# Kernel tuning notes

Hardware: AMD Instinct MI355X
Metric: run time of the kernel (lower is better)

Reference implementation:

```python
import jax, jax.numpy as jnp
import numpy as np

B, S, IN, H, Z = 8, 128, 64, 128, 64
N0, N1, N2 = B * S * S, B * (S // 2) ** 2, B * (S // 4) ** 2


def _grid(side, nb):
    # 4-neighbor grid, both edge directions, for nb stacked graphs
    idx = np.arange(side * side).reshape(side, side)
    h = np.stack([idx[:, :-1].ravel(), idx[:, 1:].ravel()])
    v = np.stack([idx[:-1, :].ravel(), idx[1:, :].ravel()])
    e = np.concatenate([h, v, h[::-1], v[::-1]], axis=1)  # [2, 4*side*(side-1)]
    return np.concatenate([e + g * side * side for g in range(nb)], axis=1)


def _cluster(side, nb):
    # 2x2 block clustering: (i,j) -> (i//2, j//2) on each graph
    i, j = np.meshgrid(np.arange(side), np.arange(side), indexing='ij')
    c = ((i // 2) * (side // 2) + (j // 2)).ravel()
    return np.concatenate([c + g * (side // 2) ** 2 for g in range(nb)])


def setup_inputs():
    ks = jax.random.split(jax.random.key(0), 16)

    def w(k, shape):
        return jax.random.normal(k, shape, jnp.float32) / np.float32(np.sqrt(shape[0]))

    return {
        'x': jax.random.normal(ks[0], (N0, IN), jnp.float32),
        'W_i1': w(ks[1], (IN, H)), 'b_i1': jnp.zeros((H,), jnp.float32),
        'W_i2': w(ks[2], (H, H)), 'b_i2': jnp.zeros((H,), jnp.float32),
        'W_b0a': w(ks[3], (H, H)), 'b_b0a': jnp.zeros((H,), jnp.float32),
        'W_b0b': w(ks[4], (H, H)), 'b_b0b': jnp.zeros((H,), jnp.float32),
        'W_b1a': w(ks[5], (H, H)), 'b_b1a': jnp.zeros((H,), jnp.float32),
        'W_b1b': w(ks[6], (H, H)), 'b_b1b': jnp.zeros((H,), jnp.float32),
        'W_mu': w(ks[7], (H, Z)), 'b_mu': jnp.zeros((Z,), jnp.float32),
        'W_lv': w(ks[8], (H, Z)), 'b_lv': jnp.zeros((Z,), jnp.float32),
        'edge_index0': jnp.asarray(_grid(S, B), jnp.int32),
        'edge_index1': jnp.asarray(_grid(S // 2, B), jnp.int32),
        'cluster0': jnp.asarray(_cluster(S, B), jnp.int32),
        'cluster1': jnp.asarray(_cluster(S // 2, B), jnp.int32),
        'batch2': jnp.asarray(np.repeat(np.arange(B), (S // 4) ** 2), jnp.int32),
    }


def _gcn(x, W, b, src, dst, n):
    # PyG GCNConv: add self-loops, symmetric D^-1/2 (A+I) D^-1/2 normalization
    h = x @ W
    loop = jnp.arange(n, dtype=src.dtype)
    s = jnp.concatenate([src, loop])
    d = jnp.concatenate([dst, loop])
    deg = jax.ops.segment_sum(jnp.ones(s.shape, x.dtype), d, num_segments=n)
    dinv = jax.lax.rsqrt(deg)  # deg >= 1 thanks to self-loops
    msg = h[s] * (dinv[s] * dinv[d])[:, None]  # [E+n, H]
    return jax.ops.segment_sum(msg, d, num_segments=n) + b


def reference(x, W_i1, b_i1, W_i2, b_i2, W_b0a, b_b0a, W_b0b, b_b0b,
              W_b1a, b_b1a, W_b1b, b_b1b, W_mu, b_mu, W_lv, b_lv,
              edge_index0, edge_index1, cluster0, cluster1, batch2):
    r = jax.nn.relu
    s0, d0 = edge_index0[0], edge_index0[1]
    h = r(_gcn(x, W_i1, b_i1, s0, d0, N0))
    h = r(_gcn(h, W_i2, b_i2, s0, d0, N0))
    # RG block 0: two GCN layers then graclus/max_pool coarsening (2x2 blocks)
    h = r(_gcn(h, W_b0a, b_b0a, s0, d0, N0))
    h = r(_gcn(h, W_b0b, b_b0b, s0, d0, N0))
    h = jax.ops.segment_max(h, cluster0, num_segments=N1)
    # RG block 1 on the coarse grid
    s1, d1 = edge_index1[0], edge_index1[1]
    h = r(_gcn(h, W_b1a, b_b1a, s1, d1, N1))
    h = r(_gcn(h, W_b1b, b_b1b, s1, d1, N1))
    h = jax.ops.segment_max(h, cluster1, num_segments=N2)
    # global mean pool per graph at the final level
    sums = jax.ops.segment_sum(h, batch2, num_segments=B)
    cnt = jax.ops.segment_sum(jnp.ones((h.shape[0], 1), h.dtype), batch2, num_segments=B)
    hg = sums / cnt  # [B, H]
    return hg @ W_mu + b_mu, hg @ W_lv + b_lv
```

## Files before the change

kernel.cpp:

```cpp
#include <hip/hip_runtime.h>
#include <hip/hip_bf16.h>
#include <stdint.h>

#define BG 8
#define HD 128
#define NN0 131072
#define NN1 32768
#define NN2 8192

typedef __attribute__((ext_vector_type(8))) _Float16 f16x8;
typedef __attribute__((ext_vector_type(4))) float f32x4;
typedef __attribute__((ext_vector_type(8))) unsigned short u16x8;

__device__ __forceinline__ float dinv_sel(int deg) {
    return deg == 3 ? 0.5773502691896258f : (deg == 4 ? 0.5f : 0.4472135954999579f);
}
template <int S>
__device__ __forceinline__ float dinv_ij(int i, int j) {
    const int deg = 1 + (i > 0) + (i < S - 1) + (j > 0) + (j < S - 1);
    return dinv_sel(deg);
}

__global__ __launch_bounds__(256) void pack_weights_kernel(
    const float* __restrict__ W0, const float* __restrict__ W1,
    const float* __restrict__ W2, const float* __restrict__ W3,
    const float* __restrict__ W4, const float* __restrict__ W5,
    _Float16* __restrict__ Wp)
{
    const int e = blockIdx.x * 256 + threadIdx.x;
    if (e >= 90112) return;
    const float* src; int off, p;
    if (e < 8192) { src = W0; off = 0; p = e; }
    else {
        const int q = e - 8192; const int w = q >> 14; p = q & 16383;
        off = 16384 + w * 32768;
        src = (w == 0) ? W1 : (w == 1) ? W2 : (w == 2) ? W3 : (w == 3) ? W4 : W5;
    }
    const int el = p & 7;
    const int lane = (p >> 3) & 63;
    const int ctkc = p >> 9;
    const int ct = ctkc & 7;
    const int kc = ctkc >> 3;
    const int k = kc * 32 + (lane >> 4) * 8 + el;
    const int col = ct * 16 + (lane & 15);
    Wp[off + p] = (_Float16)src[k * 128 + col];
}

template <int K, int SLOG, bool PRESCALE_OUT, int MODE>
__global__ __launch_bounds__(256, 4) void fused_gcn5_kernel(
    const void* __restrict__ Xv, const _Float16* __restrict__ Wa,
    const float* __restrict__ bias, _Float16* __restrict__ Hh)
{
    constexpr int S = 1 << SLOG;
    constexpr int N = BG * S * S;
    constexpr int NCH = K / 32;

    const int tid  = threadIdx.x;
    const int lane = tid & 63;
    const int wv   = tid >> 6;
    const int lr   = lane & 15;
    const int lq   = lane >> 4;

    const int bswz = ((blockIdx.x & 7) * ((int)gridDim.x >> 3)) + (blockIdx.x >> 3);
    const int n0   = bswz * 64 + wv * 16;
    const int node = n0 + lr;
    const int j = node & (S - 1);
    const int i = (node >> SLOG) & (S - 1);
    const float dvd = dinv_ij<S>(i, j);

    const int oL = (j > 0) ? -8 : 0;
    const int oR = (j < S - 1) ? 8 : 0;
    const int oU = (i > 0) ? -8 * S : 0;
    const int oD = (i < S - 1) ? 8 * S : 0;
    const float fl = (j > 0) ? 1.f : 0.f;
    const float fr = (j < S - 1) ? 1.f : 0.f;
    const float fu = (i > 0) ? 1.f : 0.f;
    const float fd = (i < S - 1) ? 1.f : 0.f;
    float w5[5];
    w5[0] = dvd;
    w5[1] = (j > 0)     ? dinv_ij<S>(i, j - 1) : 0.f;
    w5[2] = (j < S - 1) ? dinv_ij<S>(i, j + 1) : 0.f;
    w5[3] = (i > 0)     ? dinv_ij<S>(i - 1, j) : 0.f;
    w5[4] = (i < S - 1) ? dinv_ij<S>(i + 1, j) : 0.f;
    int t1o[5];
    t1o[0] = 0;
    t1o[1] = (j > 0) ? -K : 0;
    t1o[2] = (j < S - 1) ? K : 0;
    t1o[3] = (i > 0) ? -K * S : 0;
    t1o[4] = (i < S - 1) ? K * S : 0;

    f32x4 acc[8];
#pragma unroll
    for (int c = 0; c < 8; ++c) acc[c] = (f32x4){0.f, 0.f, 0.f, 0.f};

#pragma unroll
    for (int ch = 0; ch < NCH; ++ch) {
        const int q = (ch << 2) + lq;
        f16x8 bf;
        if constexpr (MODE == 0) {
            const _Float16* bp = &((const _Float16*)Xv)[((size_t)q * N + node) * 8];
            const f16x8 c8 = *reinterpret_cast<const f16x8*>(bp);
            const f16x8 l8 = *reinterpret_cast<const f16x8*>(bp + oL);
            const f16x8 r8 = *reinterpret_cast<const f16x8*>(bp + oR);
            const f16x8 u8 = *reinterpret_cast<const f16x8*>(bp + oU);
            const f16x8 d8 = *reinterpret_cast<const f16x8*>(bp + oD);
#pragma unroll
            for (int e = 0; e < 8; ++e) {
                float y = (float)c8[e];
                y = fmaf(fl, (float)l8[e], y);
                y = fmaf(fr, (float)r8[e], y);
                y = fmaf(fu, (float)u8[e], y);
                y = fmaf(fd, (float)d8[e], y);
                bf[e] = (_Float16)(y * dvd);
            }
        } else {
            const float* xb = &((const float*)Xv)[(size_t)node * K + q * 8];
            float y[8] = {0.f, 0.f, 0.f, 0.f, 0.f, 0.f, 0.f, 0.f};
#pragma unroll
            for (int t = 0; t < 5; ++t) {
                const float4 a = *reinterpret_cast<const float4*>(xb + t1o[t]);
                const float4 b = *reinterpret_cast<const float4*>(xb + t1o[t] + 4);
                const float w = w5[t];
                y[0] = fmaf(a.x, w, y[0]); y[1] = fmaf(a.y, w, y[1]);
                y[2] = fmaf(a.z, w, y[2]); y[3] = fmaf(a.w, w, y[3]);
                y[4] = fmaf(b.x, w, y[4]); y[5] = fmaf(b.y, w, y[5]);
                y[6] = fmaf(b.z, w, y[6]); y[7] = fmaf(b.w, w, y[7]);
            }
#pragma unroll
            for (int e = 0; e < 8; ++e) bf[e] = (_Float16)(y[e] * dvd);
        }
#pragma unroll
        for (int ct = 0; ct < 8; ++ct) {
            const f16x8 wf = *reinterpret_cast<const f16x8*>(
                &Wa[(size_t)(((ch << 3) + ct) * 64 + lane) * 8]);
            acc[ct] = __builtin_amdgcn_mfma_f32_16x16x32_f16(wf, bf, acc[ct], 0, 0, 0);
        }
    }

    const float dvo = PRESCALE_OUT ? dvd : 1.f;
#pragma unroll
    for (int ct = 0; ct < 8; ++ct) {
        const float4 bv = *reinterpret_cast<const float4*>(&bias[ct * 16 + lq * 4]);
        const float bb[4] = {bv.x, bv.y, bv.z, bv.w};
        union { _Float16 h[4]; uint2 u; } o;
#pragma unroll
        for (int t = 0; t < 4; ++t)
            o.h[t] = (_Float16)(fmaxf(acc[ct][t] + bb[t], 0.f) * dvo);
        const int kc2 = (ct << 1) + (lq >> 1);
        *reinterpret_cast<uint2*>(
            &Hh[((size_t)kc2 * N + node) * 8 + (lq & 1) * 4]) = o.u;
    }
}

template <int K, int SLOG, bool PRESCALE_OUT>
__global__ __launch_bounds__(256, 4) void fused_gcn_ks_kernel(
    const _Float16* __restrict__ Xp, const _Float16* __restrict__ Wa,
    const float* __restrict__ bias, _Float16* __restrict__ Hh)
{
    constexpr int S = 1 << SLOG;
    constexpr int N = BG * S * S;
    constexpr int NCH = K / 32;
    __shared__ alignas(16) float accL[2][8][64][4];

    const int tid   = threadIdx.x;
    const int lane  = tid & 63;
    const int wv    = tid >> 6;
    const int strip = wv >> 1;
    const int kh    = wv & 1;
    const int lr    = lane & 15;
    const int lq    = lane >> 4;

    const int bswz = ((blockIdx.x & 7) * ((int)gridDim.x >> 3)) + (blockIdx.x >> 3);
    const int n0   = bswz * 32 + strip * 16;
    const int node = n0 + lr;
    const int j = node & (S - 1);
    const int i = (node >> SLOG) & (S - 1);
    const float dvd = dinv_ij<S>(i, j);
    const int oL = (j > 0) ? -8 : 0;
    const int oR = (j < S - 1) ? 8 : 0;
    const int oU = (i > 0) ? -8 * S : 0;
    const int oD = (i < S - 1) ? 8 * S : 0;
    const float fl = (j > 0) ? 1.f : 0.f;
    const float fr = (j < S - 1) ? 1.f : 0.f;
    const float fu = (i > 0) ? 1.f : 0.f;
    const float fd = (i < S - 1) ? 1.f : 0.f;

    f32x4 acc[8];
#pragma unroll
    for (int c = 0; c < 8; ++c) acc[c] = (f32x4){0.f, 0.f, 0.f, 0.f};

#pragma unroll
    for (int chh = 0; chh < NCH / 2; ++chh) {
        const int ch = kh * (NCH / 2) + chh;
        const int q = (ch << 2) + lq;
        const _Float16* bp = &Xp[((size_t)q * N + node) * 8];
        const f16x8 c8 = *reinterpret_cast<const f16x8*>(bp);
        const f16x8 l8 = *reinterpret_cast<const f16x8*>(bp + oL);
        const f16x8 r8 = *reinterpret_cast<const f16x8*>(bp + oR);
        const f16x8 u8 = *reinterpret_cast<const f16x8*>(bp + oU);
        const f16x8 d8 = *reinterpret_cast<const f16x8*>(bp + oD);
        f16x8 bf;
#pragma unroll
        for (int e = 0; e < 8; ++e) {
            float y = (float)c8[e];
            y = fmaf(fl, (float)l8[e], y);
            y = fmaf(fr, (float)r8[e], y);
            y = fmaf(fu, (float)u8[e], y);
            y = fmaf(fd, (float)d8[e], y);
            bf[e] = (_Float16)(y * dvd);
        }
#pragma unroll
        for (int ct = 0; ct < 8; ++ct) {
            const f16x8 wf = *reinterpret_cast<const f16x8*>(
                &Wa[(size_t)(((ch << 3) + ct) * 64 + lane) * 8]);
            acc[ct] = __builtin_amdgcn_mfma_f32_16x16x32_f16(wf, bf, acc[ct], 0, 0, 0);
        }
    }

    if (kh == 1) {
#pragma unroll
        for (int ct = 0; ct < 8; ++ct)
            *reinterpret_cast<f32x4*>(&accL[strip][ct][lane][0]) = acc[ct];
    }
    __syncthreads();
    if (kh == 0) {
        const float dvo = PRESCALE_OUT ? dvd : 1.f;
#pragma unroll
        for (int ct = 0; ct < 8; ++ct) {
            const f32x4 p = *reinterpret_cast<const f32x4*>(&accL[strip][ct][lane][0]);
            const float4 bv = *reinterpret_cast<const float4*>(&bias[ct * 16 + lq * 4]);
            const float bb[4] = {bv.x, bv.y, bv.z, bv.w};
            union { _Float16 h[4]; uint2 u; } o;
#pragma unroll
            for (int t = 0; t < 4; ++t)
                o.h[t] = (_Float16)(fmaxf(acc[ct][t] + p[t] + bb[t], 0.f) * dvo);
            const int kc2 = (ct << 1) + (lq >> 1);
            *reinterpret_cast<uint2*>(
                &Hh[((size_t)kc2 * N + node) * 8 + (lq & 1) * 4]) = o.u;
        }
    }
}

template <int SLOG_OUT, bool SCALE>
__global__ __launch_bounds__(256) void pool_kernel(
    const _Float16* __restrict__ Hin, _Float16* __restrict__ O)
{
    constexpr int sc = 1 << SLOG_OUT;
    constexpr int Nout = BG * sc * sc;
    constexpr int Nin = Nout * 4;
    constexpr int sideIn = sc * 2;
    const int id = blockIdx.x * 256 + threadIdx.x;
    const int kc = id / Nout;
    const int n  = id & (Nout - 1);
    const int cj = n & (sc - 1);
    const int ci = (n >> SLOG_OUT) & (sc - 1);
    const int g  = n >> (2 * SLOG_OUT);
    const int nin = (g * sideIn + 2 * ci) * sideIn + 2 * cj;
    const _Float16* base = &Hin[((size_t)kc * Nin + nin) * 8];
    const u16x8 a = *reinterpret_cast<const u16x8*>(base);
    const u16x8 b = *reinterpret_cast<const u16x8*>(base + 8);
    const u16x8 c = *reinterpret_cast<const u16x8*>(base + (size_t)sideIn * 8);
    const u16x8 d = *reinterpret_cast<const u16x8*>(base + (size_t)sideIn * 8 + 8);
    u16x8 o;
#pragma unroll
    for (int e = 0; e < 8; ++e) {
        const unsigned short m1 = a[e] > b[e] ? a[e] : b[e];
        const unsigned short m2 = c[e] > d[e] ? c[e] : d[e];
        o[e] = m1 > m2 ? m1 : m2;
    }
    if (SCALE) {
        const float dv = dinv_ij<sc>(ci, cj);
#pragma unroll
        for (int e = 0; e < 8; ++e) {
            union { unsigned short u; _Float16 h; } t; t.u = o[e];
            t.h = (_Float16)((float)t.h * dv);
            o[e] = t.u;
        }
    }
    *reinterpret_cast<u16x8*>(&O[((size_t)kc * Nout + n) * 8]) = o;
}

__global__ __launch_bounds__(256) void poolmean_kernel(
    const _Float16* __restrict__ Hin, float* __restrict__ hg)
{
    __shared__ float Lp[256][8];
    const int g  = blockIdx.x >> 4;
    const int kc = blockIdx.x & 15;
    const int t  = threadIdx.x;
    float s[8] = {0.f, 0.f, 0.f, 0.f, 0.f, 0.f, 0.f, 0.f};
    const _Float16* pl = &Hin[(size_t)kc * NN1 * 8];
#pragma unroll
    for (int p = 0; p < 4; ++p) {
        const int n2 = t + (p << 8);
        const int ci = n2 >> 5, cj = n2 & 31;
        const int nf = g * 4096 + ci * 128 + cj * 2;
        const _Float16* fb = pl + (size_t)nf * 8;
        const f16x8 p00 = *reinterpret_cast<const f16x8*>(fb);
        const f16x8 p01 = *reinterpret_cast<const f16x8*>(fb + 8);
        const f16x8 p10 = *reinterpret_cast<const f16x8*>(fb + 512);
        const f16x8 p11 = *reinterpret_cast<const f16x8*>(fb + 520);
#pragma unroll
        for (int e = 0; e < 8; ++e) {
            const _Float16 m1 = p00[e] > p01[e] ? p00[e] : p01[e];
            const _Float16 m2 = p10[e] > p11[e] ? p10[e] : p11[e];
            s[e] += (float)(m1 > m2 ? m1 : m2);
        }
    }
#pragma unroll
    for (int e = 0; e < 8; ++e) Lp[t][e] = s[e];
    __syncthreads();
    for (int st = 128; st >= 1; st >>= 1) {
        if (t < st) {
#pragma unroll
            for (int e = 0; e < 8; ++e) Lp[t][e] += Lp[t + st][e];
        }
        __syncthreads();
    }
    if (t < 8) hg[g * HD + kc * 8 + t] = Lp[0][t] * (1.f / 1024.f);
}

__global__ __launch_bounds__(512) void head_kernel(
    const float* __restrict__ hg,
    const float* __restrict__ Wmu, const float* __restrict__ bmu,
    const float* __restrict__ Wlv, const float* __restrict__ blv,
    float* __restrict__ out)
{
    const int t = threadIdx.x;
    const int r = t >> 6;
    const int c = t & 63;
    float s1 = 0.f, s2 = 0.f;
#pragma unroll 8
    for (int k = 0; k < HD; ++k) {
        const float x = hg[r * HD + k];
        s1 = fmaf(x, Wmu[k * 64 + c], s1);
        s2 = fmaf(x, Wlv[k * 64 + c], s2);
    }
    out[r * 64 + c] = s1 + bmu[c];
    out[512 + r * 64 + c] = s2 + blv[c];
}

extern "C" void kernel_launch(void* const* d_in, const int* in_sizes, int n_in,
                              void* d_out, int out_size, void* d_ws, size_t ws_size,
                              hipStream_t stream) {
    const float* x     = (const float*)d_in[0];
    const float* W_i1  = (const float*)d_in[1];
    const float* b_i1  = (const float*)d_in[2];
    const float* W_i2  = (const float*)d_in[3];
    const float* b_i2  = (const float*)d_in[4];
    const float* W_b0a = (const float*)d_in[5];
    const float* b_b0a = (const float*)d_in[6];
    const float* W_b0b = (const float*)d_in[7];
    const float* b_b0b = (const float*)d_in[8];
    const float* W_b1a = (const float*)d_in[9];
    const float* b_b1a = (const float*)d_in[10];
    const float* W_b1b = (const float*)d_in[11];
    const float* b_b1b = (const float*)d_in[12];
    const float* W_mu  = (const float*)d_in[13];
    const float* b_mu  = (const float*)d_in[14];
    const float* W_lv  = (const float*)d_in[15];
    const float* b_lv  = (const float*)d_in[16];

    _Float16* Wp   = (_Float16*)d_ws;
    _Float16* bufA = (_Float16*)((char*)d_ws + 524288);
    _Float16* bufB = bufA + (size_t)NN0 * HD;
    float*    hg   = (float*)(bufB + (size_t)NN0 * HD);

    const _Float16* Wp_i1  = Wp;
    const _Float16* Wp_i2  = Wp + 16384;
    const _Float16* Wp_b0a = Wp + 16384 + 1 * 32768;
    const _Float16* Wp_b0b = Wp + 16384 + 2 * 32768;
    const _Float16* Wp_b1a = Wp + 16384 + 3 * 32768;
    const _Float16* Wp_b1b = Wp + 16384 + 4 * 32768;

    pack_weights_kernel<<<352, 256, 0, stream>>>(
        W_i1, W_i2, W_b0a, W_b0b, W_b1a, W_b1b, Wp);

    fused_gcn5_kernel<64, 7, true, 1 ><<<NN0 / 64, 256, 0, stream>>>(x,    Wp_i1,  b_i1,  bufA);
    fused_gcn5_kernel<128, 7, true, 0 ><<<NN0 / 64, 256, 0, stream>>>(bufA, Wp_i2,  b_i2,  bufB);
    fused_gcn5_kernel<128, 7, true, 0 ><<<NN0 / 64, 256, 0, stream>>>(bufB, Wp_b0a, b_b0a, bufA);
    fused_gcn5_kernel<128, 7, false, 0><<<NN0 / 64, 256, 0, stream>>>(bufA, Wp_b0b, b_b0b, bufB);

    pool_kernel<6, true><<<NN1 * 16 / 256, 256, 0, stream>>>(bufB, bufA);

    fused_gcn_ks_kernel<128, 6, true ><<<NN1 / 32, 256, 0, stream>>>(bufA, Wp_b1a, b_b1a, bufB);
    fused_gcn_ks_kernel<128, 6, false><<<NN1 / 32, 256, 0, stream>>>(bufB, Wp_b1b, b_b1b, bufA);

    poolmean_kernel<<<BG * 16, 256, 0, stream>>>(bufA, hg);

    head_kernel<<<1, 512, 0, stream>>>(hg, W_mu, b_mu, W_lv, b_lv, (float*)d_out);
}
```

Measured before the change: 129.0 us.

## Fuse 2x2 max-pool into GCN epilogues and stage weights in LDS

The last fine-grid GCN layer and the last coarse-grid layer now pool their 2x2 blocks in the epilogue. Each block's tile is remapped to two grid rows by 32 (or 16) columns so that all four pool inputs sit in the same block, and results are staged through shared memory before the max. This removes the standalone pool kernel and cuts the full-resolution intermediate writes and reads. The fine-grid kernel also copies the packed weight matrix into LDS once per block instead of reading it from global memory per wave. The risks are extra barriers and LDS pressure (32 KB for K=128), which may lower occupancy below the 4-blocks launch bound, and a changed tile order that may alter stencil-neighbour locality.

```diff
diff --git a/kernel.cpp b/kernel.cpp
--- a/kernel.cpp
+++ b/kernel.cpp
@@ -10,7 +10,6 @@
 
 typedef __attribute__((ext_vector_type(8))) _Float16 f16x8;
 typedef __attribute__((ext_vector_type(4))) float f32x4;
-typedef __attribute__((ext_vector_type(8))) unsigned short u16x8;
 
 __device__ __forceinline__ float dinv_sel(int deg) {
     return deg == 3 ? 0.5773502691896258f : (deg == 4 ? 0.5f : 0.4472135954999579f);
@@ -46,14 +45,18 @@
     Wp[off + p] = (_Float16)src[k * 128 + col];
 }
 
-template <int K, int SLOG, bool PRESCALE_OUT, int MODE>
-__global__ __launch_bounds__(256, 4) void fused_gcn5_kernel(
+template <int K, int SLOG, int MODE, bool PRESCALE_OUT, bool POOL, bool POOLSCALE>
+__global__ __launch_bounds__(256, 4) void fused_gcn6_kernel(
     const void* __restrict__ Xv, const _Float16* __restrict__ Wa,
     const float* __restrict__ bias, _Float16* __restrict__ Hh)
 {
     constexpr int S = 1 << SLOG;
     constexpr int N = BG * S * S;
     constexpr int NCH = K / 32;
+    constexpr int WCNT = K * 128;
+    constexpr int PCNT = POOL ? 4 * 16 * 136 : 0;
+    constexpr int LDSN = (WCNT > PCNT) ? WCNT : PCNT;
+    __shared__ alignas(16) _Float16 Ls[LDSN];
 
     const int tid  = threadIdx.x;
     const int lane = tid & 63;
@@ -61,11 +64,20 @@
     const int lr   = lane & 15;
     const int lq   = lane >> 4;
 
+    for (int s = tid; s < K * 16; s += 256)
+        *reinterpret_cast<uint4*>(&Ls[(size_t)s * 8]) =
+            *reinterpret_cast<const uint4*>(&Wa[(size_t)s * 8]);
+
     const int bswz = ((blockIdx.x & 7) * ((int)gridDim.x >> 3)) + (blockIdx.x >> 3);
-    const int n0   = bswz * 64 + wv * 16;
-    const int node = n0 + lr;
-    const int j = node & (S - 1);
-    const int i = (node >> SLOG) & (S - 1);
+    constexpr int TC = S / 32;
+    constexpr int TPG = (S / 2) * TC;
+    const int g0  = bswz / TPG;
+    const int rem = bswz % TPG;
+    const int r2  = rem / TC;
+    const int c32 = (rem - r2 * TC) * 32;
+    const int i   = 2 * r2 + (wv >> 1);
+    const int j   = c32 + ((wv & 1) << 4) + lr;
+    const int node = (g0 * S + i) * S + j;
     const float dvd = dinv_ij<S>(i, j);
 
     const int oL = (j > 0) ? -8 : 0;
@@ -93,6 +105,8 @@
 #pragma unroll
     for (int c = 0; c < 8; ++c) acc[c] = (f32x4){0.f, 0.f, 0.f, 0.f};
 
+    __syncthreads();
+
 #pragma unroll
     for (int ch = 0; ch < NCH; ++ch) {
         const int q = (ch << 2) + lq;
@@ -132,27 +146,66 @@
 #pragma unroll
         for (int ct = 0; ct < 8; ++ct) {
             const f16x8 wf = *reinterpret_cast<const f16x8*>(
-                &Wa[(size_t)(((ch << 3) + ct) * 64 + lane) * 8]);
+                &Ls[(size_t)(((ch << 3) + ct) * 64 + lane) * 8]);
             acc[ct] = __builtin_amdgcn_mfma_f32_16x16x32_f16(wf, bf, acc[ct], 0, 0, 0);
         }
     }
 
-    const float dvo = PRESCALE_OUT ? dvd : 1.f;
-#pragma unroll
-    for (int ct = 0; ct < 8; ++ct) {
-        const float4 bv = *reinterpret_cast<const float4*>(&bias[ct * 16 + lq * 4]);
-        const float bb[4] = {bv.x, bv.y, bv.z, bv.w};
-        union { _Float16 h[4]; uint2 u; } o;
-#pragma unroll
-        for (int t = 0; t < 4; ++t)
-            o.h[t] = (_Float16)(fmaxf(acc[ct][t] + bb[t], 0.f) * dvo);
-        const int kc2 = (ct << 1) + (lq >> 1);
-        *reinterpret_cast<uint2*>(
-            &Hh[((size_t)kc2 * N + node) * 8 + (lq & 1) * 4]) = o.u;
-    }
-}
-
-template <int K, int SLOG, bool PRESCALE_OUT>
+    if constexpr (!POOL) {
+        const float dvo = PRESCALE_OUT ? dvd : 1.f;
+#pragma unroll
+        for (int ct = 0; ct < 8; ++ct) {
+            const float4 bv = *reinterpret_cast<const float4*>(&bias[ct * 16 + lq * 4]);
+            const float bb[4] = {bv.x, bv.y, bv.z, bv.w};
+            union { _Float16 h[4]; uint2 u; } o;
+#pragma unroll
+            for (int t = 0; t < 4; ++t)
+                o.h[t] = (_Float16)(fmaxf(acc[ct][t] + bb[t], 0.f) * dvo);
+            const int kc2 = (ct << 1) + (lq >> 1);
+            *reinterpret_cast<uint2*>(
+                &Hh[((size_t)kc2 * N + node) * 8 + (lq & 1) * 4]) = o.u;
+        }
+    } else {
+        __syncthreads();
+#pragma unroll
+        for (int ct = 0; ct < 8; ++ct) {
+            const float4 bv = *reinterpret_cast<const float4*>(&bias[ct * 16 + lq * 4]);
+            const float bb[4] = {bv.x, bv.y, bv.z, bv.w};
+            union { _Float16 h[4]; uint2 u; } o;
+#pragma unroll
+            for (int t = 0; t < 4; ++t)
+                o.h[t] = (_Float16)fmaxf(acc[ct][t] + bb[t], 0.f);
+            *reinterpret_cast<uint2*>(
+                &Ls[(size_t)(wv * 16 + lr) * 136 + ct * 16 + lq * 4]) = o.u;
+        }
+        __syncthreads();
+        const int cn = tid & 15;
+        const int qq = tid >> 4;
+        const int wA = cn >> 3;
+        const int lrA = (cn << 1) & 15;
+        const _Float16* f0 = &Ls[(size_t)(wA * 16 + lrA) * 136 + qq * 8];
+        const _Float16* f2 = &Ls[(size_t)((wA + 2) * 16 + lrA) * 136 + qq * 8];
+        const f16x8 a = *reinterpret_cast<const f16x8*>(f0);
+        const f16x8 b = *reinterpret_cast<const f16x8*>(f0 + 136);
+        const f16x8 c = *reinterpret_cast<const f16x8*>(f2);
+        const f16x8 d = *reinterpret_cast<const f16x8*>(f2 + 136);
+        constexpr int S2 = S / 2;
+        const int cj2 = (c32 >> 1) + cn;
+        const float dv2 = POOLSCALE ? dinv_ij<S2>(r2, cj2) : 1.f;
+        union { _Float16 h[8]; uint4 u; } o;
+#pragma unroll
+        for (int e = 0; e < 8; ++e) {
+            const _Float16 m1 = a[e] > b[e] ? a[e] : b[e];
+            const _Float16 m2 = c[e] > d[e] ? c[e] : d[e];
+            const _Float16 m = m1 > m2 ? m1 : m2;
+            o.h[e] = POOLSCALE ? (_Float16)((float)m * dv2) : m;
+        }
+        const int nco = (g0 * S2 + r2) * S2 + cj2;
+        *reinterpret_cast<uint4*>(&Hh[((size_t)qq * (BG * S2 * S2) + nco) * 8]) = o.u;
+    }
+}
+
+template <int K, int SLOG, bool PRESCALE_OUT, bool POOL>
 __global__ __launch_bounds__(256, 4) void fused_gcn_ks_kernel(
     const _Float16* __restrict__ Xp, const _Float16* __restrict__ Wa,
     const float* __restrict__ bias, _Float16* __restrict__ Hh)
@@ -161,6 +214,7 @@
     constexpr int N = BG * S * S;
     constexpr int NCH = K / 32;
     __shared__ alignas(16) float accL[2][8][64][4];
+    __shared__ alignas(16) _Float16 fineP[POOL ? 2 * 16 * 136 : 16];
 
     const int tid   = threadIdx.x;
     const int lane  = tid & 63;
@@ -171,10 +225,15 @@
     const int lq    = lane >> 4;
 
     const int bswz = ((blockIdx.x & 7) * ((int)gridDim.x >> 3)) + (blockIdx.x >> 3);
-    const int n0   = bswz * 32 + strip * 16;
-    const int node = n0 + lr;
-    const int j = node & (S - 1);
-    const int i = (node >> SLOG) & (S - 1);
+    constexpr int TC = S / 16;
+    constexpr int TPG = (S / 2) * TC;
+    const int g0  = bswz / TPG;
+    const int rem = bswz % TPG;
+    const int r2  = rem / TC;
+    const int c16 = (rem - r2 * TC) * 16;
+    const int i   = 2 * r2 + strip;
+    const int j   = c16 + lr;
+    const int node = (g0 * S + i) * S + j;
     const float dvd = dinv_ij<S>(i, j);
     const int oL = (j > 0) ? -8 : 0;
     const int oR = (j < S - 1) ? 8 : 0;
@@ -234,53 +293,44 @@
 #pragma unroll
             for (int t = 0; t < 4; ++t)
                 o.h[t] = (_Float16)(fmaxf(acc[ct][t] + p[t] + bb[t], 0.f) * dvo);
-            const int kc2 = (ct << 1) + (lq >> 1);
-            *reinterpret_cast<uint2*>(
-                &Hh[((size_t)kc2 * N + node) * 8 + (lq & 1) * 4]) = o.u;
-        }
-    }
-}
-
-template <int SLOG_OUT, bool SCALE>
-__global__ __launch_bounds__(256) void pool_kernel(
-    const _Float16* __restrict__ Hin, _Float16* __restrict__ O)
-{
-    constexpr int sc = 1 << SLOG_OUT;
-    constexpr int Nout = BG * sc * sc;
-    constexpr int Nin = Nout * 4;
-    constexpr int sideIn = sc * 2;
-    const int id = blockIdx.x * 256 + threadIdx.x;
-    const int kc = id / Nout;
-    const int n  = id & (Nout - 1);
-    const int cj = n & (sc - 1);
-    const int ci = (n >> SLOG_OUT) & (sc - 1);
-    const int g  = n >> (2 * SLOG_OUT);
-    const int nin = (g * sideIn + 2 * ci) * sideIn + 2 * cj;
-    const _Float16* base = &Hin[((size_t)kc * Nin + nin) * 8];
-    const u16x8 a = *reinterpret_cast<const u16x8*>(base);
-    const u16x8 b = *reinterpret_cast<const u16x8*>(base + 8);
-    const u16x8 c = *reinterpret_cast<const u16x8*>(base + (size_t)sideIn * 8);
-    const u16x8 d = *reinterpret_cast<const u16x8*>(base + (size_t)sideIn * 8 + 8);
-    u16x8 o;
-#pragma unroll
-    for (int e = 0; e < 8; ++e) {
-        const unsigned short m1 = a[e] > b[e] ? a[e] : b[e];
-        const unsigned short m2 = c[e] > d[e] ? c[e] : d[e];
-        o[e] = m1 > m2 ? m1 : m2;
-    }
-    if (SCALE) {
-        const float dv = dinv_ij<sc>(ci, cj);
-#pragma unroll
-        for (int e = 0; e < 8; ++e) {
-            union { unsigned short u; _Float16 h; } t; t.u = o[e];
-            t.h = (_Float16)((float)t.h * dv);
-            o[e] = t.u;
-        }
-    }
-    *reinterpret_cast<u16x8*>(&O[((size_t)kc * Nout + n) * 8]) = o;
-}
-
-__global__ __launch_bounds__(256) void poolmean_kernel(
+            if constexpr (!POOL) {
+                const int kc2 = (ct << 1) + (lq >> 1);
+                *reinterpret_cast<uint2*>(
+                    &Hh[((size_t)kc2 * N + node) * 8 + (lq & 1) * 4]) = o.u;
+            } else {
+                *reinterpret_cast<uint2*>(
+                    &fineP[(size_t)(strip * 16 + lr) * 136 + ct * 16 + lq * 4]) = o.u;
+            }
+        }
+    }
+    if constexpr (POOL) {
+        __syncthreads();
+        if (tid < 128) {
+            const int cn = tid & 7;
+            const int qq = tid >> 3;
+            const _Float16* f0 = &fineP[(size_t)(2 * cn) * 136 + qq * 8];
+            const _Float16* f2 = &fineP[(size_t)(16 + 2 * cn) * 136 + qq * 8];
+            const f16x8 a = *reinterpret_cast<const f16x8*>(f0);
+            const f16x8 b = *reinterpret_cast<const f16x8*>(f0 + 136);
+            const f16x8 c = *reinterpret_cast<const f16x8*>(f2);
+            const f16x8 d = *reinterpret_cast<const f16x8*>(f2 + 136);
+            union { _Float16 h[8]; uint4 u; } o;
+#pragma unroll
+            for (int e = 0; e < 8; ++e) {
+                const _Float16 m1 = a[e] > b[e] ? a[e] : b[e];
+                const _Float16 m2 = c[e] > d[e] ? c[e] : d[e];
+                o.h[e] = m1 > m2 ? m1 : m2;
+            }
+            constexpr int S2 = S / 2;
+            const int cj2 = (c16 >> 1) + cn;
+            const int nco = (g0 * S2 + r2) * S2 + cj2;
+            *reinterpret_cast<uint4*>(
+                &Hh[((size_t)qq * (BG * S2 * S2) + nco) * 8]) = o.u;
+        }
+    }
+}
+
+__global__ __launch_bounds__(256) void mean_kernel(
     const _Float16* __restrict__ Hin, float* __restrict__ hg)
 {
     __shared__ float Lp[256][8];
@@ -288,23 +338,13 @@
     const int kc = blockIdx.x & 15;
     const int t  = threadIdx.x;
     float s[8] = {0.f, 0.f, 0.f, 0.f, 0.f, 0.f, 0.f, 0.f};
-    const _Float16* pl = &Hin[(size_t)kc * NN1 * 8];
 #pragma unroll
     for (int p = 0; p < 4; ++p) {
-        const int n2 = t + (p << 8);
-        const int ci = n2 >> 5, cj = n2 & 31;
-        const int nf = g * 4096 + ci * 128 + cj * 2;
-        const _Float16* fb = pl + (size_t)nf * 8;
-        const f16x8 p00 = *reinterpret_cast<const f16x8*>(fb);
-        const f16x8 p01 = *reinterpret_cast<const f16x8*>(fb + 8);
-        const f16x8 p10 = *reinterpret_cast<const f16x8*>(fb + 512);
-        const f16x8 p11 = *reinterpret_cast<const f16x8*>(fb + 520);
-#pragma unroll
-        for (int e = 0; e < 8; ++e) {
-            const _Float16 m1 = p00[e] > p01[e] ? p00[e] : p01[e];
-            const _Float16 m2 = p10[e] > p11[e] ? p10[e] : p11[e];
-            s[e] += (float)(m1 > m2 ? m1 : m2);
-        }
+        const int n = g * 1024 + t + (p << 8);
+        const f16x8 v = *reinterpret_cast<const f16x8*>(
+            &Hin[((size_t)kc * NN2 + n) * 8]);
+#pragma unroll
+        for (int e = 0; e < 8; ++e) s[e] += (float)v[e];
     }
 #pragma unroll
     for (int e = 0; e < 8; ++e) Lp[t][e] = s[e];
@@ -375,17 +415,21 @@
     pack_weights_kernel<<<352, 256, 0, stream>>>(
         W_i1, W_i2, W_b0a, W_b0b, W_b1a, W_b1b, Wp);
 
-    fused_gcn5_kernel<64, 7, true, 1 ><<<NN0 / 64, 256, 0, stream>>>(x,    Wp_i1,  b_i1,  bufA);
-    fused_gcn5_kernel<128, 7, true, 0 ><<<NN0 / 64, 256, 0, stream>>>(bufA, Wp_i2,  b_i2,  bufB);
-    fused_gcn5_kernel<128, 7, true, 0 ><<<NN0 / 64, 256, 0, stream>>>(bufB, Wp_b0a, b_b0a, bufA);
-    fused_gcn5_kernel<128, 7, false, 0><<<NN0 / 64, 256, 0, stream>>>(bufA, Wp_b0b, b_b0b, bufB);
-
-    pool_kernel<6, true><<<NN1 * 16 / 256, 256, 0, stream>>>(bufB, bufA);
-
-    fused_gcn_ks_kernel<128, 6, true ><<<NN1 / 32, 256, 0, stream>>>(bufA, Wp_b1a, b_b1a, bufB);
-    fused_gcn_ks_kernel<128, 6, false><<<NN1 / 32, 256, 0, stream>>>(bufB, Wp_b1b, b_b1b, bufA);
-
-    poolmean_kernel<<<BG * 16, 256, 0, stream>>>(bufA, hg);
+    fused_gcn6_kernel<64, 7, 1, true, false, false>
+        <<<NN0 / 64, 256, 0, stream>>>(x, Wp_i1, b_i1, bufA);
+    fused_gcn6_kernel<128, 7, 0, true, false, false>
+        <<<NN0 / 64, 256, 0, stream>>>(bufA, Wp_i2, b_i2, bufB);
+    fused_gcn6_kernel<128, 7, 0, true, false, false>
+        <<<NN0 / 64, 256, 0, stream>>>(bufB, Wp_b0a, b_b0a, bufA);
+    fused_gcn6_kernel<128, 7, 0, false, true, true>
+        <<<NN0 / 64, 256, 0, stream>>>(bufA, Wp_b0b, b_b0b, bufB);
+
+    fused_gcn_ks_kernel<128, 6, true, false>
+        <<<NN1 / 32, 256, 0, stream>>>(bufB, Wp_b1a, b_b1a, bufA);
+    fused_gcn_ks_kernel<128, 6, false, true>
+        <<<NN1 / 32, 256, 0, stream>>>(bufA, Wp_b1b, b_b1b, bufB);
+
+    mean_kernel<<<BG * 16, 256, 0, stream>>>(bufB, hg);
 
     head_kernel<<<1, 512, 0, stream>>>(hg, W_mu, b_mu, W_lv, b_lv, (float*)d_out);
 }
```

Result: faster. 111.8 us (-13.3%).
